# Kernel tuning notes

Hardware: AMD Instinct MI355X
Metric: run time of the kernel (lower is better)

The kernel has to match this reference:

```python
import jax, jax.numpy as jnp
import numpy as np
from itertools import product

C0, C1, C_IN, C_OUT = 16, 32, 1, 32
GRID = 768

def _enc(c):
    # injective int64 hash of 3D integer coords (values in [-4, 2043])
    return ((c[:, 0] + 4) * 2048 + (c[:, 1] + 4)) * 2048 + (c[:, 2] + 4)

def _build_km(coords, offsets):
    # kernel map for a stride-1 conv on one coordinate set:
    # per kernel offset o, pairs (in_idx, out_idx) with coords[in] == coords[out] + o
    N = coords.shape[0]
    keys = _enc(coords)
    order = np.argsort(keys)
    skeys = keys[order]
    ins, outs = [], []
    for o in offsets:
        qk = _enc(coords + np.asarray(o, np.int64))
        pos = np.searchsorted(skeys, qk)
        posc = np.clip(pos, 0, N - 1)
        valid = skeys[posc] == qk
        ins.append(order[posc[valid]].astype(np.int32))
        outs.append(np.nonzero(valid)[0].astype(np.int32))
    P = max(len(a) for a in ins)
    km_in = np.full((len(offsets), P), N, np.int32)   # pad -> zero row of x
    km_out = np.full((len(offsets), P), N, np.int32)  # pad -> dropped out row
    for k in range(len(offsets)):
        km_in[k, :len(ins[k])] = ins[k]
        km_out[k, :len(outs[k])] = outs[k]
    return km_in, km_out

def setup_inputs() -> dict:
    # voxelized surface heightfield: realistic sparse 3D point cloud occupancy
    xs, ys = np.meshgrid(np.arange(GRID), np.arange(GRID), indexing='ij')
    z = np.round(40.0 * np.sin(xs / 24.0) + 40.0 * np.cos(ys / 24.0)).astype(np.int64) + 128
    coords0 = np.stack([xs.ravel(), ys.ravel(), z.ravel()], 1).astype(np.int64)
    n0 = coords0.shape[0]
    offs27 = list(product((-1, 0, 1), repeat=3))
    km0_in, km0_out = _build_km(coords0, offs27)

    # stride-2 kernel-2 downsample: out coord = floor(c/2), offset = c mod 2
    u2 = coords0 // 2
    coords1, inv = np.unique(u2, axis=0, return_inverse=True)
    inv = inv.reshape(-1)
    n1 = coords1.shape[0]
    o = coords0 - 2 * u2
    kk = o[:, 0] * 4 + o[:, 1] * 2 + o[:, 2]
    ins, outs = [], []
    for k in range(8):
        m = np.nonzero(kk == k)[0]
        ins.append(m.astype(np.int32))
        outs.append(inv[m].astype(np.int32))
    P = max(len(a) for a in ins)
    kmd_in = np.full((8, P), n0, np.int32)
    kmd_out = np.full((8, P), n1, np.int32)
    for k in range(8):
        kmd_in[k, :len(ins[k])] = ins[k]
        kmd_out[k, :len(outs[k])] = outs[k]

    km1_in, km1_out = _build_km(coords1, offs27)

    key = jax.random.key(0)
    ks = jax.random.split(key, 6)
    w = lambda k, sh: jax.random.normal(k, sh, jnp.float32) * 0.1
    z32 = lambda c: jnp.zeros((c,), jnp.float32)
    return dict(
        in_feats=jnp.ones((n0, C_IN), jnp.float32),
        W_first=w(ks[0], (27, C_IN, C0)), b_first=z32(C0),
        W_pre=w(ks[1], (27, C0, C0)), b_pre=z32(C0),
        W_down=w(ks[2], (8, C0, C1)), b_down=z32(C1),
        W_r0=w(ks[3], (27, C1, C1)), b_r0=z32(C1),
        W_r1=w(ks[4], (27, C1, C1)), b_r1=z32(C1),
        W_fin=w(ks[5], (27, C1, C_OUT)), b_fin=z32(C_OUT),
        km0_in=jnp.asarray(km0_in), km0_out=jnp.asarray(km0_out),
        kmd_in=jnp.asarray(kmd_in), kmd_out=jnp.asarray(kmd_out),
        km1_in=jnp.asarray(km1_in), km1_out=jnp.asarray(km1_out),
        n1=int(n1),
    )

def _sparse_conv(x, W, b, km_in, km_out, n_out):
    # gather-GEMM-scatter sparse conv: out[j] += x[i] @ W[k] over pairs of offset k
    xp = jnp.concatenate([x, jnp.zeros((1, x.shape[1]), x.dtype)], 0)
    out = jnp.zeros((n_out + 1, W.shape[-1]), x.dtype)
    for k in range(W.shape[0]):  # static small loop over kernel offsets
        out = out.at[km_out[k]].add(xp[km_in[k]] @ W[k])
    return out[:n_out] + b

def reference(in_feats, W_first, b_first, W_pre, b_pre, W_down, b_down,
              W_r0, b_r0, W_r1, b_r1, W_fin, b_fin,
              km0_in, km0_out, kmd_in, kmd_out, km1_in, km1_out, n1):
    n0 = in_feats.shape[0]
    relu = jax.nn.relu
    # first_block: 3^3 conv + relu
    x = relu(_sparse_conv(in_feats, W_first, b_first, km0_in, km0_out, n0))
    cached = x  # cached_feature_list[0] (use_skip_connection=False)
    # blocks[0]: conv3x3 + relu, stride-2 downsample conv + relu
    x = relu(_sparse_conv(x, W_pre, b_pre, km0_in, km0_out, n0))
    x = relu(_sparse_conv(x, W_down, b_down, kmd_in, kmd_out, n1))
    # ResBlock
    r = relu(_sparse_conv(x, W_r0, b_r0, km1_in, km1_out, n1))
    r = _sparse_conv(r, W_r1, b_r1, km1_in, km1_out, n1)
    x = r + x
    # final conv (act=None)
    out = _sparse_conv(x, W_fin, b_fin, km1_in, km1_out, n1)
    return (out, cached)
```

## Files before the change

### kernel.cpp

```cpp
#include <hip/hip_runtime.h>


#define TPB 256

typedef __attribute__((ext_vector_type(8))) short short8;
typedef __attribute__((ext_vector_type(4))) float floatx4;

static __device__ __forceinline__ unsigned short f2b(float f) {
    union { float f; unsigned u; } v; v.f = f;
    unsigned r = v.u + 0x7fffu + ((v.u >> 16) & 1u);
    return (unsigned short)(r >> 16);
}
static __device__ __forceinline__ float b2f(unsigned short h) {
    union { unsigned u; float f; } v; v.u = ((unsigned)h) << 16;
    return v.f;
}

__global__ void search_k(const int* __restrict__ km0_out,
                         const int* __restrict__ km1_out,
                         long long P0, long long P1, int T0, int T1,
                         int n0, int n1,
                         int* __restrict__ st0, int* __restrict__ st1) {
    unsigned t = blockIdx.x * blockDim.x + threadIdx.x;
    unsigned N0 = 27u * (unsigned)(T0 + 1);
    unsigned N1 = 27u * (unsigned)(T1 + 1);
    const int* row;
    long long P;
    int th;
    int* dst;
    if (t < N0) {
        unsigned k = t / (unsigned)(T0 + 1), tile = t - k * (unsigned)(T0 + 1);
        row = km0_out + (long long)k * P0; P = P0;
        long long thr = (long long)tile * 64;
        th = thr < n0 ? (int)thr : n0;
        dst = st0 + t;
    } else {
        t -= N0;
        if (t >= N1) return;
        unsigned k = t / (unsigned)(T1 + 1), tile = t - k * (unsigned)(T1 + 1);
        row = km1_out + (long long)k * P1; P = P1;
        long long thr = (long long)tile * 64;
        th = thr < n1 ? (int)thr : n1;
        dst = st1 + t;
    }
    long long lo = 0, hi = P;
    while (lo < hi) {
        long long mid = (lo + hi) >> 1;
        if (row[mid] < th) lo = mid + 1; else hi = mid;
    }
    *dst = (int)lo;
}

static __device__ __forceinline__ void pack16_elem(
    const float* __restrict__ W, unsigned short* __restrict__ Wp,
    int t, int COUT, int Ksrc) {
    int j = t & 7;
    int r = t >> 3;
    int n = r % COUT; r /= COUT;
    int q = r & 3;
    int k2 = r >> 2;
    int ks = 2 * k2 + (q >> 1);
    int cin = (q & 1) * 8 + j;
    float v = (ks < Ksrc) ? W[(ks * 16 + cin) * COUT + n] : 0.f;
    Wp[t] = f2b(v);
}

__global__ void prep_all(const int* __restrict__ kmd_in, const int* __restrict__ kmd_out,
                         int* __restrict__ td, unsigned Pd, unsigned rc1, unsigned n1,
                         const float* __restrict__ W_pre, const float* __restrict__ W_down,
                         const float* __restrict__ W_r0, const float* __restrict__ W_r1,
                         const float* __restrict__ W_fin,
                         unsigned short* __restrict__ wp_pre, unsigned short* __restrict__ wp_down,
                         unsigned short* __restrict__ wp_r0, unsigned short* __restrict__ wp_r1,
                         unsigned short* __restrict__ wp_fin,
                         unsigned short* p0, unsigned short* p1, unsigned short* p2,
                         unsigned short* p3, unsigned short* p4) {
    unsigned tu = blockIdx.x * blockDim.x + threadIdx.x;
    unsigned Nd = 8u * Pd;
    if (tu < Nd) {
        int o = kmd_out[tu];
        int i = kmd_in[tu];
        if ((unsigned)o < n1) td[(tu / Pd) * rc1 + (unsigned)o] = i;
        return;
    }
    int t = (int)(tu - Nd);
    if (t < 7168) { pack16_elem(W_pre, wp_pre, t, 16, 27); return; }
    t -= 7168;
    if (t < 4096) { pack16_elem(W_down, wp_down, t, 32, 8); return; }
    t -= 4096;
    if (t < 27648) {
        int j = t & 7, n = (t >> 3) & 31, q = (t >> 8) & 3, k = t >> 10;
        wp_r0[t] = f2b(W_r0[(k * 32 + q * 8 + j) * 32 + n]); return;
    }
    t -= 27648;
    if (t < 27648) {
        int j = t & 7, n = (t >> 3) & 31, q = (t >> 8) & 3, k = t >> 10;
        wp_r1[t] = f2b(W_r1[(k * 32 + q * 8 + j) * 32 + n]); return;
    }
    t -= 27648;
    if (t < 27648) {
        int j = t & 7, n = (t >> 3) & 31, q = (t >> 8) & 3, k = t >> 10;
        wp_fin[t] = f2b(W_fin[(k * 32 + q * 8 + j) * 32 + n]); return;
    }
    t -= 27648;
    if (t < 16) p0[t] = 0;
    else if (t < 32) p1[t - 16] = 0;
    else if (t < 64) p2[t - 32] = 0;
    else if (t < 96) p3[t - 64] = 0;
    else if (t < 128) p4[t - 96] = 0;
}

__global__ __launch_bounds__(TPB) void conv_first_k(
    const float* __restrict__ xin, const float* __restrict__ W,
    const float* __restrict__ b,
    const int* __restrict__ km_in, const int* __restrict__ km_out,
    const int* __restrict__ st, long long P, int T,
    int n0, float* __restrict__ outf, unsigned short* __restrict__ outb) {
    __shared__ int lidx[27][256];
    const int blk = (int)blockIdx.x;
    const int j0 = blk * 256;
    const int wv = (int)(threadIdx.x >> 6), lane = (int)(threadIdx.x & 63);
    const int ta = 4 * blk;
    const int tb = (4 * blk + 4 < T) ? 4 * blk + 4 : T;
    for (int r = wv; r < 27; r += 4) {
#pragma unroll
        for (int i = 0; i < 4; ++i) lidx[r][lane + 64 * i] = n0;
        int s = st[r * (T + 1) + ta];
        int e = st[r * (T + 1) + tb];
        for (int i = s + lane; i < e; i += 64) {
            int o = km_out[(long long)r * P + i];
            lidx[r][o - j0] = km_in[(long long)r * P + i];
        }
    }
    __syncthreads();
    int j = j0 + (int)threadIdx.x;
    if (j >= n0) return;
    float acc[16];
#pragma unroll
    for (int c = 0; c < 16; ++c) acc[c] = b[c];
#pragma unroll
    for (int k = 0; k < 27; ++k) {
        int idx = lidx[k][threadIdx.x];
        bool ok = idx < n0;
        int cidx = ok ? idx : 0;
        float v = xin[cidx];
        v = ok ? v : 0.f;
        const float* Wk = W + k * 16;
#pragma unroll
        for (int c = 0; c < 16; ++c) acc[c] = fmaf(v, Wk[c], acc[c]);
    }
    float* orow = outf + (long long)j * 16;
    unsigned short* brow = outb + (long long)j * 16;
#pragma unroll
    for (int c = 0; c < 16; ++c) {
        float v = fmaxf(acc[c], 0.f);
        orow[c] = v;
        brow[c] = f2b(v);
    }
}

template <int CIN, int COUT, int NT, int SB, int SE, bool CSR>
static __device__ __forceinline__ void kchunk(
    const unsigned short* __restrict__ xb, const unsigned short* __restrict__ Wp,
    const int* __restrict__ tab, long long rowcap, const int* lidx, int n_in,
    long long j0, int m, int q, int coff, floatx4 (&acc)[4][NT]) {
    constexpr int NS = SE - SB;
    if (NS <= 0) return;
    int idx[NS > 0 ? NS : 1][4];
#pragma unroll
    for (int s = 0; s < NS; ++s) {
        const int ks = (CIN == 32) ? (SB + s) : 2 * (SB + s) + (q >> 1);
#pragma unroll
        for (int t = 0; t < 4; ++t) {
            if (CSR) {
                idx[s][t] = lidx[ks * 64 + 16 * t + m];
            } else {
                const int* trow = tab + (long long)ks * rowcap + j0 + m;
                unsigned v = (unsigned)trow[16 * t];
                idx[s][t] = (int)(v < (unsigned)n_in ? v : (unsigned)n_in);
            }
        }
    }
    short8 cur[4];
#pragma unroll
    for (int t = 0; t < 4; ++t)
        cur[t] = *(const short8*)(xb + (long long)idx[0][t] * CIN + coff);
#pragma unroll
    for (int s = 0; s < NS; ++s) {
        short8 nxt[4];
        if (s + 1 < NS) {
#pragma unroll
            for (int t = 0; t < 4; ++t)
                nxt[t] = *(const short8*)(xb + (long long)idx[s + 1][t] * CIN + coff);
        }
        short8 b0 = *(const short8*)(Wp + ((((SB + s) * 4 + q) * COUT) + m) * 8);
        short8 b1;
        if (NT == 2) b1 = *(const short8*)(Wp + ((((SB + s) * 4 + q) * COUT) + 16 + m) * 8);
#pragma unroll
        for (int t = 0; t < 4; ++t) {
            acc[t][0] = __builtin_amdgcn_mfma_f32_16x16x32_bf16(cur[t], b0, acc[t][0], 0, 0, 0);
            if (NT == 2)
                acc[t][1] = __builtin_amdgcn_mfma_f32_16x16x32_bf16(cur[t], b1, acc[t][1], 0, 0, 0);
        }
        if (s + 1 < NS) {
#pragma unroll
            for (int t = 0; t < 4; ++t) cur[t] = nxt[t];
        }
    }
}

template <int CIN, int COUT, int NT, int SB, int SE, bool CSR>
static __device__ __forceinline__ void chunk_run(
    const unsigned short* __restrict__ xb, const unsigned short* __restrict__ Wp,
    const int* __restrict__ km_in, const int* __restrict__ km_out,
    const int* __restrict__ st, int T, long long P,
    const int* __restrict__ tab, long long rowcap,
    int n_in, long long j0, int tile, int lane, int m, int q, int coff,
    int* lidx, floatx4 (&acc)[4][NT]) {
    if (CSR) {
        constexpr int R0 = (CIN == 32) ? SB : 2 * SB;
        constexpr int R1 = (CIN == 32) ? SE : 2 * SE;
#pragma unroll
        for (int r = R0; r < R1; ++r) lidx[r * 64 + lane] = n_in;
#pragma unroll
        for (int r = R0; r < R1; ++r) {
            if (r < 27) {
                int s = st[r * (T + 1) + tile];
                int e = st[r * (T + 1) + tile + 1];
                int i = s + lane;
                if (i < e) {
                    int o = km_out[(long long)r * P + i];
                    lidx[r * 64 + (o - (int)j0)] = km_in[(long long)r * P + i];
                }
            }
        }
    }
    kchunk<CIN, COUT, NT, SB, SE, CSR>(xb, Wp, tab, rowcap, lidx, n_in,
                                       CSR ? 0 : j0, m, q, coff, acc);
}

template <int CIN, int COUT, int STEPS, bool CSR, bool RELU, bool RES, bool WF32, bool WB16>
__global__ __launch_bounds__(TPB, 4) void conv_mfma(
    const unsigned short* __restrict__ xb,
    const unsigned short* __restrict__ Wp,
    const float* __restrict__ bias,
    const int* __restrict__ km_in, const int* __restrict__ km_out,
    const int* __restrict__ st, int T, long long P,
    const int* __restrict__ tab, long long rowcap,
    int n_in, int n_out, long long ntiles,
    const unsigned short* __restrict__ resb,
    float* __restrict__ outf, unsigned short* __restrict__ outb) {
    constexpr int NT = COUT / 16;
    constexpr int NR = (CIN == 16) ? 2 * STEPS : STEPS;
    __shared__ floatx4 red[NT][12 * 64];
    __shared__ int lidx[CSR ? NR * 64 : 64];
    int runs = (int)gridDim.x >> 3;
    long long tile = (long long)((blockIdx.x & 7) * runs + (blockIdx.x >> 3));
    if (tile >= ntiles) return;
    int wv = (int)((threadIdx.x >> 6) & 3);
    int lane = (int)threadIdx.x & 63;
    int m = lane & 15, q = lane >> 4;
    long long j0 = tile * 64;

    floatx4 acc[4][NT];
#pragma unroll
    for (int t = 0; t < 4; ++t)
#pragma unroll
        for (int nt = 0; nt < NT; ++nt) acc[t][nt] = floatx4{0.f, 0.f, 0.f, 0.f};

    const int coff = (CIN == 32) ? q * 8 : (q & 1) * 8;
    constexpr int C1 = STEPS / 4, C2 = STEPS / 2, C3 = (3 * STEPS) / 4;
    if (wv == 0)
        chunk_run<CIN, COUT, NT, 0, C1, CSR>(xb, Wp, km_in, km_out, st, T, P, tab, rowcap,
                                             n_in, j0, (int)tile, lane, m, q, coff, lidx, acc);
    else if (wv == 1)
        chunk_run<CIN, COUT, NT, C1, C2, CSR>(xb, Wp, km_in, km_out, st, T, P, tab, rowcap,
                                              n_in, j0, (int)tile, lane, m, q, coff, lidx, acc);
    else if (wv == 2)
        chunk_run<CIN, COUT, NT, C2, C3, CSR>(xb, Wp, km_in, km_out, st, T, P, tab, rowcap,
                                              n_in, j0, (int)tile, lane, m, q, coff, lidx, acc);
    else
        chunk_run<CIN, COUT, NT, C3, STEPS, CSR>(xb, Wp, km_in, km_out, st, T, P, tab, rowcap,
                                                 n_in, j0, (int)tile, lane, m, q, coff, lidx, acc);

#pragma unroll
    for (int t = 0; t < 4; ++t) {
        if (t != wv) {
            int sl = wv * 3 + (t > wv ? t - 1 : t);
#pragma unroll
            for (int nt = 0; nt < NT; ++nt)
                red[nt][sl * 64 + lane] = acc[t][nt];
        }
    }
    floatx4 own[NT];
#pragma unroll
    for (int nt = 0; nt < NT; ++nt) own[nt] = acc[0][nt];
#pragma unroll
    for (int t = 1; t < 4; ++t)
#pragma unroll
        for (int nt = 0; nt < NT; ++nt)
            if (wv == t) own[nt] = acc[t][nt];
    __syncthreads();
#pragma unroll
    for (int w = 0; w < 4; ++w) {
        if (w != wv) {
            int sl = w * 3 + (wv > w ? wv - 1 : wv);
#pragma unroll
            for (int nt = 0; nt < NT; ++nt)
                own[nt] += red[nt][sl * 64 + lane];
        }
    }

    float bs[2];
    bs[0] = bias[m];
    if (NT == 2) bs[1] = bias[16 + m];
    long long jb = j0 + wv * 16;
#pragma unroll
    for (int u = 0; u < 4; ++u) {
        long long r = jb + q * 4 + u;
        if (r < n_out) {
#pragma unroll
            for (int nt = 0; nt < NT; ++nt) {
                float v = own[nt][u] + bs[nt];
                if (RES) v += b2f(resb[r * COUT + nt * 16 + m]);
                if (RELU) v = fmaxf(v, 0.f);
                if (WF32) outf[r * COUT + nt * 16 + m] = v;
                if (WB16) outb[r * COUT + nt * 16 + m] = f2b(v);
            }
        }
    }
}

static inline unsigned nblk(long long n, int b) { return (unsigned)((n + b - 1) / b); }
static inline unsigned pad8(unsigned g) { return ((g + 7) / 8) * 8; }
static inline size_t align64(size_t x) { return (x + 63) & ~(size_t)63; }

extern "C" void kernel_launch(void* const* d_in, const int* in_sizes, int n_in_cnt,
                              void* d_out, int out_size, void* d_ws, size_t ws_size,
                              hipStream_t stream) {
    const float* in_feats = (const float*)d_in[0];
    const float* W_first = (const float*)d_in[1];
    const float* b_first = (const float*)d_in[2];
    const float* W_pre   = (const float*)d_in[3];
    const float* b_pre   = (const float*)d_in[4];
    const float* W_down  = (const float*)d_in[5];
    const float* b_down  = (const float*)d_in[6];
    const float* W_r0    = (const float*)d_in[7];
    const float* b_r0    = (const float*)d_in[8];
    const float* W_r1    = (const float*)d_in[9];
    const float* b_r1    = (const float*)d_in[10];
    const float* W_fin   = (const float*)d_in[11];
    const float* b_fin   = (const float*)d_in[12];
    const int* km0_in  = (const int*)d_in[13];
    const int* km0_out = (const int*)d_in[14];
    const int* kmd_in  = (const int*)d_in[15];
    const int* kmd_out = (const int*)d_in[16];
    const int* km1_in  = (const int*)d_in[17];
    const int* km1_out = (const int*)d_in[18];

    const int n0 = in_sizes[0];
    const int n1 = (out_size - 16 * n0) / 32;
    const long long P0 = in_sizes[13] / 27;
    const long long Pd = in_sizes[15] / 8;
    const long long P1 = in_sizes[17] / 27;

    const long long rc1 = ((n1 + 64) / 64) * 64;
    const long long rc0 = ((n0 + 64) / 64) * 64;
    const int T0 = (int)(rc0 / 64), T1 = (int)(rc1 / 64);

    float* out_lo = (float*)d_out;
    float* cached = out_lo + (size_t)n1 * 32;

    char* base = (char*)d_ws;
    size_t off = 0;
    auto alloc = [&](size_t bytes) { void* p = base + off; off = align64(off + bytes); return p; };
    int* td = (int*)alloc(sizeof(int) * 8 * rc1);
    int* st0 = (int*)alloc(sizeof(int) * 27 * (T0 + 1));
    int* st1 = (int*)alloc(sizeof(int) * 27 * (T1 + 1));
    unsigned short* c0b   = (unsigned short*)alloc(sizeof(short) * 16 * (n0 + 1));
    unsigned short* x0pre = (unsigned short*)alloc(sizeof(short) * 16 * (n0 + 1));
    unsigned short* x1a   = (unsigned short*)alloc(sizeof(short) * 32 * (n1 + 1));
    unsigned short* x1b   = (unsigned short*)alloc(sizeof(short) * 32 * (n1 + 1));
    unsigned short* x1c   = (unsigned short*)alloc(sizeof(short) * 32 * (n1 + 1));
    unsigned short* wp_pre  = (unsigned short*)alloc(sizeof(short) * 14 * 4 * 16 * 8);
    unsigned short* wp_down = (unsigned short*)alloc(sizeof(short) * 4 * 4 * 32 * 8);
    unsigned short* wp_r0   = (unsigned short*)alloc(sizeof(short) * 27 * 1024);
    unsigned short* wp_r1   = (unsigned short*)alloc(sizeof(short) * 27 * 1024);
    unsigned short* wp_fin  = (unsigned short*)alloc(sizeof(short) * 27 * 1024);
    (void)ws_size; (void)n_in_cnt;

    const long long searchN = 27LL * (T0 + 1) + 27LL * (T1 + 1);
    search_k<<<nblk(searchN, TPB), TPB, 0, stream>>>(
        km0_out, km1_out, P0, P1, T0, T1, n0, n1, st0, st1);

    const long long prepN = 8 * Pd + 7168 + 4096 + 3 * 27648 + 128;
    prep_all<<<nblk(prepN, TPB), TPB, 0, stream>>>(
        kmd_in, kmd_out, td, (unsigned)Pd, (unsigned)rc1, (unsigned)n1,
        W_pre, W_down, W_r0, W_r1, W_fin,
        wp_pre, wp_down, wp_r0, wp_r1, wp_fin,
        c0b + (size_t)n0 * 16, x0pre + (size_t)n0 * 16,
        x1a + (size_t)n1 * 32, x1b + (size_t)n1 * 32, x1c + (size_t)n1 * 32);

    conv_first_k<<<nblk(n0, TPB), TPB, 0, stream>>>(
        in_feats, W_first, b_first, km0_in, km0_out, st0, P0, T0, n0, cached, c0b);

    const unsigned g0 = pad8((unsigned)T0), g1 = pad8((unsigned)T1);
    conv_mfma<16, 16, 14, true, true, false, false, true><<<g0, TPB, 0, stream>>>(
        c0b, wp_pre, b_pre, km0_in, km0_out, st0, T0, P0, nullptr, 0,
        n0, n0, T0, nullptr, nullptr, x0pre);
    conv_mfma<16, 32, 4, false, true, false, false, true><<<g1, TPB, 0, stream>>>(
        x0pre, wp_down, b_down, nullptr, nullptr, nullptr, 0, 0, td, rc1,
        n0, n1, T1, nullptr, nullptr, x1a);
    conv_mfma<32, 32, 27, true, true, false, false, true><<<g1, TPB, 0, stream>>>(
        x1a, wp_r0, b_r0, km1_in, km1_out, st1, T1, P1, nullptr, 0,
        n1, n1, T1, nullptr, nullptr, x1b);
    conv_mfma<32, 32, 27, true, false, true, false, true><<<g1, TPB, 0, stream>>>(
        x1b, wp_r1, b_r1, km1_in, km1_out, st1, T1, P1, nullptr, 0,
        n1, n1, T1, x1a, nullptr, x1c);
    conv_mfma<32, 32, 27, true, false, false, true, false><<<g1, TPB, 0, stream>>>(
        x1c, wp_fin, b_fin, km1_in, km1_out, st1, T1, P1, nullptr, 0,
        n1, n1, T1, nullptr, out_lo, nullptr);
}
```

Before: 471.3 us.

## Stage per-tile input bands in LDS and split waves by output rows

The CSR convolution kernels now compute, for each 64-row output tile, the min/max input index within each of three kernel-offset groups. When a group's span fits in 160 rows, those input feature rows are copied into a swizzled LDS band, and the gathers read from LDS instead of global memory, with a per-step fallback to global. Work is also re-split so each wave owns 16 output rows across all kernel steps, which removes the cross-wave LDS reduction. The downsample conv moves to its own specialized kernel. This adds several block barriers, atomics and LDS staging, and loses the software prefetch of the next step's gathers.

```diff
diff --git a/kernel.cpp b/kernel.cpp
--- a/kernel.cpp
+++ b/kernel.cpp
@@ -159,101 +159,164 @@
     }
 }
 
-template <int CIN, int COUT, int NT, int SB, int SE, bool CSR>
-static __device__ __forceinline__ void kchunk(
-    const unsigned short* __restrict__ xb, const unsigned short* __restrict__ Wp,
-    const int* __restrict__ tab, long long rowcap, const int* lidx, int n_in,
-    long long j0, int m, int q, int coff, floatx4 (&acc)[4][NT]) {
-    constexpr int NS = SE - SB;
-    if (NS <= 0) return;
-    int idx[NS > 0 ? NS : 1][4];
-#pragma unroll
-    for (int s = 0; s < NS; ++s) {
-        const int ks = (CIN == 32) ? (SB + s) : 2 * (SB + s) + (q >> 1);
-#pragma unroll
-        for (int t = 0; t < 4; ++t) {
-            if (CSR) {
-                idx[s][t] = lidx[ks * 64 + 16 * t + m];
-            } else {
-                const int* trow = tab + (long long)ks * rowcap + j0 + m;
-                unsigned v = (unsigned)trow[16 * t];
-                idx[s][t] = (int)(v < (unsigned)n_in ? v : (unsigned)n_in);
-            }
-        }
-    }
-    short8 cur[4];
-#pragma unroll
-    for (int t = 0; t < 4; ++t)
-        cur[t] = *(const short8*)(xb + (long long)idx[0][t] * CIN + coff);
-#pragma unroll
-    for (int s = 0; s < NS; ++s) {
-        short8 nxt[4];
-        if (s + 1 < NS) {
-#pragma unroll
-            for (int t = 0; t < 4; ++t)
-                nxt[t] = *(const short8*)(xb + (long long)idx[s + 1][t] * CIN + coff);
-        }
-        short8 b0 = *(const short8*)(Wp + ((((SB + s) * 4 + q) * COUT) + m) * 8);
-        short8 b1;
-        if (NT == 2) b1 = *(const short8*)(Wp + ((((SB + s) * 4 + q) * COUT) + 16 + m) * 8);
-#pragma unroll
-        for (int t = 0; t < 4; ++t) {
-            acc[t][0] = __builtin_amdgcn_mfma_f32_16x16x32_bf16(cur[t], b0, acc[t][0], 0, 0, 0);
-            if (NT == 2)
-                acc[t][1] = __builtin_amdgcn_mfma_f32_16x16x32_bf16(cur[t], b1, acc[t][1], 0, 0, 0);
-        }
-        if (s + 1 < NS) {
-#pragma unroll
-            for (int t = 0; t < 4; ++t) cur[t] = nxt[t];
-        }
-    }
-}
-
-template <int CIN, int COUT, int NT, int SB, int SE, bool CSR>
-static __device__ __forceinline__ void chunk_run(
-    const unsigned short* __restrict__ xb, const unsigned short* __restrict__ Wp,
-    const int* __restrict__ km_in, const int* __restrict__ km_out,
-    const int* __restrict__ st, int T, long long P,
-    const int* __restrict__ tab, long long rowcap,
-    int n_in, long long j0, int tile, int lane, int m, int q, int coff,
-    int* lidx, floatx4 (&acc)[4][NT]) {
-    if (CSR) {
-        constexpr int R0 = (CIN == 32) ? SB : 2 * SB;
-        constexpr int R1 = (CIN == 32) ? SE : 2 * SE;
-#pragma unroll
-        for (int r = R0; r < R1; ++r) lidx[r * 64 + lane] = n_in;
-#pragma unroll
-        for (int r = R0; r < R1; ++r) {
-            if (r < 27) {
-                int s = st[r * (T + 1) + tile];
-                int e = st[r * (T + 1) + tile + 1];
-                int i = s + lane;
-                if (i < e) {
-                    int o = km_out[(long long)r * P + i];
-                    lidx[r * 64 + (o - (int)j0)] = km_in[(long long)r * P + i];
-                }
-            }
-        }
-    }
-    kchunk<CIN, COUT, NT, SB, SE, CSR>(xb, Wp, tab, rowcap, lidx, n_in,
-                                       CSR ? 0 : j0, m, q, coff, acc);
-}
-
-template <int CIN, int COUT, int STEPS, bool CSR, bool RELU, bool RES, bool WF32, bool WB16>
-__global__ __launch_bounds__(TPB, 4) void conv_mfma(
+template <int CIN, int COUT, int STEPS, bool RELU, bool RES, bool WF32, bool WB16>
+__global__ __launch_bounds__(TPB, 4) void conv_band(
     const unsigned short* __restrict__ xb,
     const unsigned short* __restrict__ Wp,
     const float* __restrict__ bias,
     const int* __restrict__ km_in, const int* __restrict__ km_out,
     const int* __restrict__ st, int T, long long P,
-    const int* __restrict__ tab, long long rowcap,
     int n_in, int n_out, long long ntiles,
     const unsigned short* __restrict__ resb,
     float* __restrict__ outf, unsigned short* __restrict__ outb) {
     constexpr int NT = COUT / 16;
-    constexpr int NR = (CIN == 16) ? 2 * STEPS : STEPS;
-    __shared__ floatx4 red[NT][12 * 64];
-    __shared__ int lidx[CSR ? NR * 64 : 64];
+    constexpr int NK = (CIN == 16) ? 2 * STEPS : STEPS;
+    constexpr int NS16 = (CIN * 2) / 16;
+    constexpr int CAP = 160;
+    constexpr int ZROW = 3 * CAP;
+    __shared__ short8 bandmem8[((3 * CAP + 1) * CIN) / 8];
+    unsigned short* bandmem = (unsigned short*)bandmem8;
+    __shared__ int lidx[NK * 64];
+    __shared__ int blo[3], bhi[3];
+    __shared__ int fbstep[STEPS];
+
+    int runs = (int)gridDim.x >> 3;
+    long long tile = (long long)((blockIdx.x & 7) * runs + (blockIdx.x >> 3));
+    if (tile >= ntiles) return;
+    const int tid = (int)threadIdx.x;
+    const int wv = tid >> 6;
+    const int lane = tid & 63;
+    const int m = lane & 15, q = lane >> 4;
+    const int qr = (CIN == 32) ? q : (q & 1);
+    const long long j0 = tile * 64;
+
+    if (tid < 3) { blo[tid] = 0x7fffffff; bhi[tid] = -1; }
+    if (tid < CIN / 2) ((unsigned*)(bandmem + ZROW * CIN))[tid] = 0u;
+    __syncthreads();
+
+    {
+        int k = tid >> 3;
+        if (k < 27) {
+            int s = st[k * (T + 1) + (int)tile];
+            int e = st[k * (T + 1) + (int)tile + 1];
+            int g = k / 9;
+            int lmin = 0x7fffffff, lmax = -1;
+            for (int i = s + (tid & 7); i < e; i += 8) {
+                int v = km_in[(long long)k * P + i];
+                lmin = v < lmin ? v : lmin;
+                lmax = v > lmax ? v : lmax;
+            }
+            if (lmax >= 0) { atomicMin(&blo[g], lmin); atomicMax(&bhi[g], lmax); }
+        }
+    }
+    __syncthreads();
+
+    if (tid < STEPS) {
+        int k0 = (CIN == 32) ? tid : 2 * tid;
+        int g0 = k0 / 9;
+        bool fb = ((long long)bhi[g0] - blo[g0] + 1) > CAP;
+        if (CIN == 16) {
+            int k1 = 2 * tid + 1;
+            if (k1 < 27) {
+                int g1 = k1 / 9;
+                fb = fb || (((long long)bhi[g1] - blo[g1] + 1) > CAP);
+            }
+        }
+        fbstep[tid] = fb ? 1 : 0;
+    }
+    for (int g = 0; g < 3; ++g) {
+        int lo = blo[g];
+        long long w = (long long)bhi[g] - lo + 1;
+        if (w <= 0 || w > CAP) continue;
+        int qs = tid & (NS16 - 1);
+        for (int r = tid / NS16; r < (int)w; r += TPB / NS16) {
+            int R = g * CAP + r;
+            int slot = qs ^ (R & (NS16 - 1));
+            *(short8*)(bandmem + R * CIN + slot * 8) =
+                *(const short8*)(xb + (long long)(lo + r) * CIN + qs * 8);
+        }
+    }
+    __syncthreads();
+
+    for (int x = tid; x < NK * 64; x += TPB) {
+        int k = x >> 6;
+        int sidx = (CIN == 32) ? k : (k >> 1);
+        lidx[x] = fbstep[sidx] ? n_in : ZROW;
+    }
+    __syncthreads();
+
+    {
+        int k = tid >> 3;
+        if (k < 27) {
+            int s = st[k * (T + 1) + (int)tile];
+            int e = st[k * (T + 1) + (int)tile + 1];
+            int g = k / 9;
+            int sidx = (CIN == 32) ? k : (k >> 1);
+            int fb = fbstep[sidx];
+            int lo = blo[g];
+            for (int i = s + (tid & 7); i < e; i += 8) {
+                int o = km_out[(long long)k * P + i];
+                int gi = km_in[(long long)k * P + i];
+                lidx[k * 64 + (o - (int)j0)] = fb ? gi : (g * CAP + (gi - lo));
+            }
+        }
+    }
+    __syncthreads();
+
+    floatx4 acc[NT];
+#pragma unroll
+    for (int nt = 0; nt < NT; ++nt) acc[nt] = floatx4{0.f, 0.f, 0.f, 0.f};
+
+    int lv[STEPS];
+#pragma unroll
+    for (int s = 0; s < STEPS; ++s) {
+        const int ks = (CIN == 32) ? s : 2 * s + (q >> 1);
+        lv[s] = lidx[ks * 64 + wv * 16 + m];
+    }
+#pragma unroll
+    for (int s = 0; s < STEPS; ++s) {
+        short8 a;
+        if (fbstep[s]) {
+            a = *(const short8*)(xb + (long long)lv[s] * CIN + qr * 8);
+        } else {
+            int R = lv[s];
+            int slot = qr ^ (R & (NS16 - 1));
+            a = *(const short8*)(bandmem + R * CIN + slot * 8);
+        }
+        short8 b0 = *(const short8*)(Wp + (((s * 4 + q) * COUT) + m) * 8);
+        acc[0] = __builtin_amdgcn_mfma_f32_16x16x32_bf16(a, b0, acc[0], 0, 0, 0);
+        if (NT == 2) {
+            short8 b1 = *(const short8*)(Wp + (((s * 4 + q) * COUT) + 16 + m) * 8);
+            acc[1] = __builtin_amdgcn_mfma_f32_16x16x32_bf16(a, b1, acc[1], 0, 0, 0);
+        }
+    }
+
+    float bs[2];
+    bs[0] = bias[m];
+    if (NT == 2) bs[1] = bias[16 + m];
+    long long jb = j0 + wv * 16;
+#pragma unroll
+    for (int u = 0; u < 4; ++u) {
+        long long r = jb + q * 4 + u;
+        if (r < n_out) {
+#pragma unroll
+            for (int nt = 0; nt < NT; ++nt) {
+                float v = acc[nt][u] + bs[nt];
+                if (RES) v += b2f(resb[r * COUT + nt * 16 + m]);
+                if (RELU) v = fmaxf(v, 0.f);
+                if (WF32) outf[r * COUT + nt * 16 + m] = v;
+                if (WB16) outb[r * COUT + nt * 16 + m] = f2b(v);
+            }
+        }
+    }
+}
+
+__global__ __launch_bounds__(TPB, 4) void conv_down_k(
+    const unsigned short* __restrict__ xb, const unsigned short* __restrict__ Wp,
+    const float* __restrict__ bias,
+    const int* __restrict__ tab, long long rowcap, int n_in, int n_out,
+    long long ntiles, unsigned short* __restrict__ outb) {
+    __shared__ floatx4 red[2][12 * 64];
     int runs = (int)gridDim.x >> 3;
     long long tile = (long long)((blockIdx.x & 7) * runs + (blockIdx.x >> 3));
     if (tile >= ntiles) return;
@@ -262,71 +325,62 @@
     int m = lane & 15, q = lane >> 4;
     long long j0 = tile * 64;
 
-    floatx4 acc[4][NT];
-#pragma unroll
-    for (int t = 0; t < 4; ++t)
-#pragma unroll
-        for (int nt = 0; nt < NT; ++nt) acc[t][nt] = floatx4{0.f, 0.f, 0.f, 0.f};
-
-    const int coff = (CIN == 32) ? q * 8 : (q & 1) * 8;
-    constexpr int C1 = STEPS / 4, C2 = STEPS / 2, C3 = (3 * STEPS) / 4;
-    if (wv == 0)
-        chunk_run<CIN, COUT, NT, 0, C1, CSR>(xb, Wp, km_in, km_out, st, T, P, tab, rowcap,
-                                             n_in, j0, (int)tile, lane, m, q, coff, lidx, acc);
-    else if (wv == 1)
-        chunk_run<CIN, COUT, NT, C1, C2, CSR>(xb, Wp, km_in, km_out, st, T, P, tab, rowcap,
-                                              n_in, j0, (int)tile, lane, m, q, coff, lidx, acc);
-    else if (wv == 2)
-        chunk_run<CIN, COUT, NT, C2, C3, CSR>(xb, Wp, km_in, km_out, st, T, P, tab, rowcap,
-                                              n_in, j0, (int)tile, lane, m, q, coff, lidx, acc);
-    else
-        chunk_run<CIN, COUT, NT, C3, STEPS, CSR>(xb, Wp, km_in, km_out, st, T, P, tab, rowcap,
-                                                 n_in, j0, (int)tile, lane, m, q, coff, lidx, acc);
-
+    floatx4 acc[4][2];
+#pragma unroll
+    for (int t = 0; t < 4; ++t) { acc[t][0] = floatx4{0,0,0,0}; acc[t][1] = floatx4{0,0,0,0}; }
+
+    const int coff = (q & 1) * 8;
+    const int s = wv;
+    {
+        const int ks = 2 * s + (q >> 1);
+        const int* trow = tab + (long long)ks * rowcap + j0 + m;
+        int idx[4];
+#pragma unroll
+        for (int t = 0; t < 4; ++t) {
+            unsigned v = (unsigned)trow[16 * t];
+            idx[t] = (int)(v < (unsigned)n_in ? v : (unsigned)n_in);
+        }
+        short8 b0 = *(const short8*)(Wp + (((s * 4 + q) * 32) + m) * 8);
+        short8 b1 = *(const short8*)(Wp + (((s * 4 + q) * 32) + 16 + m) * 8);
+#pragma unroll
+        for (int t = 0; t < 4; ++t) {
+            short8 a = *(const short8*)(xb + (long long)idx[t] * 16 + coff);
+            acc[t][0] = __builtin_amdgcn_mfma_f32_16x16x32_bf16(a, b0, acc[t][0], 0, 0, 0);
+            acc[t][1] = __builtin_amdgcn_mfma_f32_16x16x32_bf16(a, b1, acc[t][1], 0, 0, 0);
+        }
+    }
 #pragma unroll
     for (int t = 0; t < 4; ++t) {
         if (t != wv) {
             int sl = wv * 3 + (t > wv ? t - 1 : t);
-#pragma unroll
-            for (int nt = 0; nt < NT; ++nt)
-                red[nt][sl * 64 + lane] = acc[t][nt];
-        }
-    }
-    floatx4 own[NT];
-#pragma unroll
-    for (int nt = 0; nt < NT; ++nt) own[nt] = acc[0][nt];
+            red[0][sl * 64 + lane] = acc[t][0];
+            red[1][sl * 64 + lane] = acc[t][1];
+        }
+    }
+    floatx4 own[2];
+    own[0] = acc[0][0]; own[1] = acc[0][1];
 #pragma unroll
     for (int t = 1; t < 4; ++t)
-#pragma unroll
-        for (int nt = 0; nt < NT; ++nt)
-            if (wv == t) own[nt] = acc[t][nt];
+        if (wv == t) { own[0] = acc[t][0]; own[1] = acc[t][1]; }
     __syncthreads();
 #pragma unroll
     for (int w = 0; w < 4; ++w) {
         if (w != wv) {
             int sl = w * 3 + (wv > w ? wv - 1 : wv);
-#pragma unroll
-            for (int nt = 0; nt < NT; ++nt)
-                own[nt] += red[nt][sl * 64 + lane];
-        }
-    }
-
-    float bs[2];
-    bs[0] = bias[m];
-    if (NT == 2) bs[1] = bias[16 + m];
+            own[0] += red[0][sl * 64 + lane];
+            own[1] += red[1][sl * 64 + lane];
+        }
+    }
+    float bs0 = bias[m], bs1 = bias[16 + m];
     long long jb = j0 + wv * 16;
 #pragma unroll
     for (int u = 0; u < 4; ++u) {
         long long r = jb + q * 4 + u;
         if (r < n_out) {
-#pragma unroll
-            for (int nt = 0; nt < NT; ++nt) {
-                float v = own[nt][u] + bs[nt];
-                if (RES) v += b2f(resb[r * COUT + nt * 16 + m]);
-                if (RELU) v = fmaxf(v, 0.f);
-                if (WF32) outf[r * COUT + nt * 16 + m] = v;
-                if (WB16) outb[r * COUT + nt * 16 + m] = f2b(v);
-            }
+            float v0 = fmaxf(own[0][u] + bs0, 0.f);
+            float v1 = fmaxf(own[1][u] + bs1, 0.f);
+            outb[r * 32 + m] = f2b(v0);
+            outb[r * 32 + 16 + m] = f2b(v1);
         }
     }
 }
@@ -405,19 +459,18 @@
         in_feats, W_first, b_first, km0_in, km0_out, st0, P0, T0, n0, cached, c0b);
 
     const unsigned g0 = pad8((unsigned)T0), g1 = pad8((unsigned)T1);
-    conv_mfma<16, 16, 14, true, true, false, false, true><<<g0, TPB, 0, stream>>>(
-        c0b, wp_pre, b_pre, km0_in, km0_out, st0, T0, P0, nullptr, 0,
+    conv_band<16, 16, 14, true, false, false, true><<<g0, TPB, 0, stream>>>(
+        c0b, wp_pre, b_pre, km0_in, km0_out, st0, T0, P0,
         n0, n0, T0, nullptr, nullptr, x0pre);
-    conv_mfma<16, 32, 4, false, true, false, false, true><<<g1, TPB, 0, stream>>>(
-        x0pre, wp_down, b_down, nullptr, nullptr, nullptr, 0, 0, td, rc1,
-        n0, n1, T1, nullptr, nullptr, x1a);
-    conv_mfma<32, 32, 27, true, true, false, false, true><<<g1, TPB, 0, stream>>>(
-        x1a, wp_r0, b_r0, km1_in, km1_out, st1, T1, P1, nullptr, 0,
+    conv_down_k<<<g1, TPB, 0, stream>>>(
+        x0pre, wp_down, b_down, td, rc1, n0, n1, T1, x1a);
+    conv_band<32, 32, 27, true, false, false, true><<<g1, TPB, 0, stream>>>(
+        x1a, wp_r0, b_r0, km1_in, km1_out, st1, T1, P1,
         n1, n1, T1, nullptr, nullptr, x1b);
-    conv_mfma<32, 32, 27, true, false, true, false, true><<<g1, TPB, 0, stream>>>(
-        x1b, wp_r1, b_r1, km1_in, km1_out, st1, T1, P1, nullptr, 0,
+    conv_band<32, 32, 27, false, true, false, true><<<g1, TPB, 0, stream>>>(
+        x1b, wp_r1, b_r1, km1_in, km1_out, st1, T1, P1,
         n1, n1, T1, x1a, nullptr, x1c);
-    conv_mfma<32, 32, 27, true, false, false, true, false><<<g1, TPB, 0, stream>>>(
-        x1c, wp_fin, b_fin, km1_in, km1_out, st1, T1, P1, nullptr, 0,
+    conv_band<32, 32, 27, false, false, true, false><<<g1, TPB, 0, stream>>>(
+        x1c, wp_fin, b_fin, km1_in, km1_out, st1, T1, P1,
         n1, n1, T1, nullptr, out_lo, nullptr);
 }
```

Result: slower. 586.3 us (+24.4%).

## Precompute dense gather tables once instead of rebuilding CSR maps per conv

Applied to the files above, without the earlier changes.

Adds a tabgen kernel that scatters the sorted kernel maps into dense per-offset index tables (one for level 0, one for level 1) once. The first conv and all MFMA convs then read indices directly from these tables rather than each block rebuilding a shared-memory index map from km_in/km_out on every layer. This removes repeated CSR scatter work, its syncs and the shared-memory footprint. In exchange it adds a kernel launch and extra global table traffic.

```diff
diff --git a/kernel.cpp b/kernel.cpp
--- a/kernel.cpp
+++ b/kernel.cpp
@@ -51,6 +51,40 @@
     *dst = (int)lo;
 }
 
+__global__ __launch_bounds__(TPB) void tabgen(
+    const int* __restrict__ km0_in, const int* __restrict__ km0_out,
+    const int* __restrict__ km1_in, const int* __restrict__ km1_out,
+    const int* __restrict__ st0, const int* __restrict__ st1,
+    int* __restrict__ t0, int* __restrict__ t1,
+    long long P0, long long P1, int T0, int T1, int n0, int n1) {
+    __shared__ int slots[TPB];
+    const int w = (int)blockIdx.y;
+    const int* kin; const int* kout; const int* st; int* tab;
+    long long P; int T, n, k;
+    if (w < 27) { k = w;      kin = km0_in; kout = km0_out; st = st0; tab = t0; P = P0; T = T0; n = n0; }
+    else        { k = w - 27; kin = km1_in; kout = km1_out; st = st1; tab = t1; P = P1; T = T1; n = n1; }
+    const int tile0 = (int)blockIdx.x * 4;
+    if (tile0 >= T) return;
+    const int tid = (int)threadIdx.x;
+    const int wv = tid >> 6, lane = tid & 63;
+    slots[tid] = n;
+    __syncthreads();
+    const int tile = tile0 + wv;
+    if (tile < T) {
+        int s = st[k * (T + 1) + tile];
+        int e = st[k * (T + 1) + tile + 1];
+        if (s + lane < e) {
+            int o = kout[(long long)k * P + s + lane];
+            int i = kin[(long long)k * P + s + lane];
+            slots[wv * 64 + (o - tile * 64)] = i;
+        }
+    }
+    __syncthreads();
+    const long long rc = (long long)T * 64;
+    long long slot = (long long)tile0 * 64 + tid;
+    if (slot < rc) tab[(long long)k * rc + slot] = slots[tid];
+}
+
 static __device__ __forceinline__ void pack16_elem(
     const float* __restrict__ W, unsigned short* __restrict__ Wp,
     int t, int COUT, int Ksrc) {
@@ -112,36 +146,17 @@
 
 __global__ __launch_bounds__(TPB) void conv_first_k(
     const float* __restrict__ xin, const float* __restrict__ W,
-    const float* __restrict__ b,
-    const int* __restrict__ km_in, const int* __restrict__ km_out,
-    const int* __restrict__ st, long long P, int T,
+    const float* __restrict__ b, const int* __restrict__ tab, long long rowcap,
     int n0, float* __restrict__ outf, unsigned short* __restrict__ outb) {
-    __shared__ int lidx[27][256];
-    const int blk = (int)blockIdx.x;
-    const int j0 = blk * 256;
-    const int wv = (int)(threadIdx.x >> 6), lane = (int)(threadIdx.x & 63);
-    const int ta = 4 * blk;
-    const int tb = (4 * blk + 4 < T) ? 4 * blk + 4 : T;
-    for (int r = wv; r < 27; r += 4) {
-#pragma unroll
-        for (int i = 0; i < 4; ++i) lidx[r][lane + 64 * i] = n0;
-        int s = st[r * (T + 1) + ta];
-        int e = st[r * (T + 1) + tb];
-        for (int i = s + lane; i < e; i += 64) {
-            int o = km_out[(long long)r * P + i];
-            lidx[r][o - j0] = km_in[(long long)r * P + i];
-        }
-    }
-    __syncthreads();
-    int j = j0 + (int)threadIdx.x;
+    int j = blockIdx.x * blockDim.x + threadIdx.x;
     if (j >= n0) return;
     float acc[16];
 #pragma unroll
     for (int c = 0; c < 16; ++c) acc[c] = b[c];
 #pragma unroll
     for (int k = 0; k < 27; ++k) {
-        int idx = lidx[k][threadIdx.x];
-        bool ok = idx < n0;
+        int idx = tab[(long long)k * rowcap + j];
+        bool ok = (unsigned)idx < (unsigned)n0;
         int cidx = ok ? idx : 0;
         float v = xin[cidx];
         v = ok ? v : 0.f;
@@ -159,10 +174,10 @@
     }
 }
 
-template <int CIN, int COUT, int NT, int SB, int SE, bool CSR>
+template <int CIN, int COUT, int NT, int SB, int SE>
 static __device__ __forceinline__ void kchunk(
     const unsigned short* __restrict__ xb, const unsigned short* __restrict__ Wp,
-    const int* __restrict__ tab, long long rowcap, const int* lidx, int n_in,
+    const int* __restrict__ tab, long long rowcap, int n_in,
     long long j0, int m, int q, int coff, floatx4 (&acc)[4][NT]) {
     constexpr int NS = SE - SB;
     if (NS <= 0) return;
@@ -170,15 +185,11 @@
 #pragma unroll
     for (int s = 0; s < NS; ++s) {
         const int ks = (CIN == 32) ? (SB + s) : 2 * (SB + s) + (q >> 1);
+        const int* trow = tab + (long long)ks * rowcap + j0 + m;
 #pragma unroll
         for (int t = 0; t < 4; ++t) {
-            if (CSR) {
-                idx[s][t] = lidx[ks * 64 + 16 * t + m];
-            } else {
-                const int* trow = tab + (long long)ks * rowcap + j0 + m;
-                unsigned v = (unsigned)trow[16 * t];
-                idx[s][t] = (int)(v < (unsigned)n_in ? v : (unsigned)n_in);
-            }
+            unsigned v = (unsigned)trow[16 * t];
+            idx[s][t] = (int)(v < (unsigned)n_in ? v : (unsigned)n_in);
         }
     }
     short8 cur[4];
@@ -209,51 +220,17 @@
     }
 }
 
-template <int CIN, int COUT, int NT, int SB, int SE, bool CSR>
-static __device__ __forceinline__ void chunk_run(
-    const unsigned short* __restrict__ xb, const unsigned short* __restrict__ Wp,
-    const int* __restrict__ km_in, const int* __restrict__ km_out,
-    const int* __restrict__ st, int T, long long P,
-    const int* __restrict__ tab, long long rowcap,
-    int n_in, long long j0, int tile, int lane, int m, int q, int coff,
-    int* lidx, floatx4 (&acc)[4][NT]) {
-    if (CSR) {
-        constexpr int R0 = (CIN == 32) ? SB : 2 * SB;
-        constexpr int R1 = (CIN == 32) ? SE : 2 * SE;
-#pragma unroll
-        for (int r = R0; r < R1; ++r) lidx[r * 64 + lane] = n_in;
-#pragma unroll
-        for (int r = R0; r < R1; ++r) {
-            if (r < 27) {
-                int s = st[r * (T + 1) + tile];
-                int e = st[r * (T + 1) + tile + 1];
-                int i = s + lane;
-                if (i < e) {
-                    int o = km_out[(long long)r * P + i];
-                    lidx[r * 64 + (o - (int)j0)] = km_in[(long long)r * P + i];
-                }
-            }
-        }
-    }
-    kchunk<CIN, COUT, NT, SB, SE, CSR>(xb, Wp, tab, rowcap, lidx, n_in,
-                                       CSR ? 0 : j0, m, q, coff, acc);
-}
-
-template <int CIN, int COUT, int STEPS, bool CSR, bool RELU, bool RES, bool WF32, bool WB16>
+template <int CIN, int COUT, int STEPS, bool RELU, bool RES, bool WF32, bool WB16>
 __global__ __launch_bounds__(TPB, 4) void conv_mfma(
     const unsigned short* __restrict__ xb,
     const unsigned short* __restrict__ Wp,
     const float* __restrict__ bias,
-    const int* __restrict__ km_in, const int* __restrict__ km_out,
-    const int* __restrict__ st, int T, long long P,
-    const int* __restrict__ tab, long long rowcap,
-    int n_in, int n_out, long long ntiles,
+    const int* __restrict__ tab, long long rowcap, int n_in, int n_out,
+    long long ntiles,
     const unsigned short* __restrict__ resb,
     float* __restrict__ outf, unsigned short* __restrict__ outb) {
     constexpr int NT = COUT / 16;
-    constexpr int NR = (CIN == 16) ? 2 * STEPS : STEPS;
     __shared__ floatx4 red[NT][12 * 64];
-    __shared__ int lidx[CSR ? NR * 64 : 64];
     int runs = (int)gridDim.x >> 3;
     long long tile = (long long)((blockIdx.x & 7) * runs + (blockIdx.x >> 3));
     if (tile >= ntiles) return;
@@ -271,17 +248,13 @@
     const int coff = (CIN == 32) ? q * 8 : (q & 1) * 8;
     constexpr int C1 = STEPS / 4, C2 = STEPS / 2, C3 = (3 * STEPS) / 4;
     if (wv == 0)
-        chunk_run<CIN, COUT, NT, 0, C1, CSR>(xb, Wp, km_in, km_out, st, T, P, tab, rowcap,
-                                             n_in, j0, (int)tile, lane, m, q, coff, lidx, acc);
+        kchunk<CIN, COUT, NT, 0, C1>(xb, Wp, tab, rowcap, n_in, j0, m, q, coff, acc);
     else if (wv == 1)
-        chunk_run<CIN, COUT, NT, C1, C2, CSR>(xb, Wp, km_in, km_out, st, T, P, tab, rowcap,
-                                              n_in, j0, (int)tile, lane, m, q, coff, lidx, acc);
+        kchunk<CIN, COUT, NT, C1, C2>(xb, Wp, tab, rowcap, n_in, j0, m, q, coff, acc);
     else if (wv == 2)
-        chunk_run<CIN, COUT, NT, C2, C3, CSR>(xb, Wp, km_in, km_out, st, T, P, tab, rowcap,
-                                              n_in, j0, (int)tile, lane, m, q, coff, lidx, acc);
+        kchunk<CIN, COUT, NT, C2, C3>(xb, Wp, tab, rowcap, n_in, j0, m, q, coff, acc);
     else
-        chunk_run<CIN, COUT, NT, C3, STEPS, CSR>(xb, Wp, km_in, km_out, st, T, P, tab, rowcap,
-                                                 n_in, j0, (int)tile, lane, m, q, coff, lidx, acc);
+        kchunk<CIN, COUT, NT, C3, STEPS>(xb, Wp, tab, rowcap, n_in, j0, m, q, coff, acc);
 
 #pragma unroll
     for (int t = 0; t < 4; ++t) {
@@ -364,8 +337,8 @@
     const long long Pd = in_sizes[15] / 8;
     const long long P1 = in_sizes[17] / 27;
 
+    const long long rc0 = ((n0 + 64) / 64) * 64;
     const long long rc1 = ((n1 + 64) / 64) * 64;
-    const long long rc0 = ((n0 + 64) / 64) * 64;
     const int T0 = (int)(rc0 / 64), T1 = (int)(rc1 / 64);
 
     float* out_lo = (float*)d_out;
@@ -374,6 +347,8 @@
     char* base = (char*)d_ws;
     size_t off = 0;
     auto alloc = [&](size_t bytes) { void* p = base + off; off = align64(off + bytes); return p; };
+    int* t0 = (int*)alloc(sizeof(int) * 28 * rc0);
+    int* t1 = (int*)alloc(sizeof(int) * 27 * rc1);
     int* td = (int*)alloc(sizeof(int) * 8 * rc1);
     int* st0 = (int*)alloc(sizeof(int) * 27 * (T0 + 1));
     int* st1 = (int*)alloc(sizeof(int) * 27 * (T1 + 1));
@@ -393,6 +368,13 @@
     search_k<<<nblk(searchN, TPB), TPB, 0, stream>>>(
         km0_out, km1_out, P0, P1, T0, T1, n0, n1, st0, st1);
 
+    {
+        int Tm = T0 > T1 ? T0 : T1;
+        dim3 tg(nblk(Tm, 4), 54);
+        tabgen<<<tg, TPB, 0, stream>>>(km0_in, km0_out, km1_in, km1_out,
+                                       st0, st1, t0, t1, P0, P1, T0, T1, n0, n1);
+    }
+
     const long long prepN = 8 * Pd + 7168 + 4096 + 3 * 27648 + 128;
     prep_all<<<nblk(prepN, TPB), TPB, 0, stream>>>(
         kmd_in, kmd_out, td, (unsigned)Pd, (unsigned)rc1, (unsigned)n1,
@@ -401,23 +383,17 @@
         c0b + (size_t)n0 * 16, x0pre + (size_t)n0 * 16,
         x1a + (size_t)n1 * 32, x1b + (size_t)n1 * 32, x1c + (size_t)n1 * 32);
 
-    conv_first_k<<<nblk(n0, TPB), TPB, 0, stream>>>(
-        in_feats, W_first, b_first, km0_in, km0_out, st0, P0, T0, n0, cached, c0b);
-
+    conv_first_k<<<nblk(n0, TPB), TPB, 0, stream>>>(in_feats, W_first, b_first, t0, rc0,
+                                                    n0, cached, c0b);
     const unsigned g0 = pad8((unsigned)T0), g1 = pad8((unsigned)T1);
-    conv_mfma<16, 16, 14, true, true, false, false, true><<<g0, TPB, 0, stream>>>(
-        c0b, wp_pre, b_pre, km0_in, km0_out, st0, T0, P0, nullptr, 0,
-        n0, n0, T0, nullptr, nullptr, x0pre);
-    conv_mfma<16, 32, 4, false, true, false, false, true><<<g1, TPB, 0, stream>>>(
-        x0pre, wp_down, b_down, nullptr, nullptr, nullptr, 0, 0, td, rc1,
-        n0, n1, T1, nullptr, nullptr, x1a);
-    conv_mfma<32, 32, 27, true, true, false, false, true><<<g1, TPB, 0, stream>>>(
-        x1a, wp_r0, b_r0, km1_in, km1_out, st1, T1, P1, nullptr, 0,
-        n1, n1, T1, nullptr, nullptr, x1b);
-    conv_mfma<32, 32, 27, true, false, true, false, true><<<g1, TPB, 0, stream>>>(
-        x1b, wp_r1, b_r1, km1_in, km1_out, st1, T1, P1, nullptr, 0,
-        n1, n1, T1, x1a, nullptr, x1c);
-    conv_mfma<32, 32, 27, true, false, false, true, false><<<g1, TPB, 0, stream>>>(
-        x1c, wp_fin, b_fin, km1_in, km1_out, st1, T1, P1, nullptr, 0,
-        n1, n1, T1, nullptr, out_lo, nullptr);
-}
+    conv_mfma<16, 16, 14, true, false, false, true><<<g0, TPB, 0, stream>>>(
+        c0b, wp_pre, b_pre, t0, rc0, n0, n0, T0, nullptr, nullptr, x0pre);
+    conv_mfma<16, 32, 4, true, false, false, true><<<g1, TPB, 0, stream>>>(
+        x0pre, wp_down, b_down, td, rc1, n0, n1, T1, nullptr, nullptr, x1a);
+    conv_mfma<32, 32, 27, true, false, false, true><<<g1, TPB, 0, stream>>>(
+        x1a, wp_r0, b_r0, t1, rc1, n1, n1, T1, nullptr, nullptr, x1b);
+    conv_mfma<32, 32, 27, false, true, false, true><<<g1, TPB, 0, stream>>>(
+        x1b, wp_r1, b_r1, t1, rc1, n1, n1, T1, x1a, nullptr, x1c);
+    conv_mfma<32, 32, 27, false, false, true, false><<<g1, TPB, 0, stream>>>(
+        x1c, wp_fin, b_fin, t1, rc1, n1, n1, T1, nullptr, out_lo, nullptr);
+}
```

After: 512.2 us. +8.7%, slower.
